# Optimization experiments

Hardware: AMD Instinct MI355X
Metric: run time of the kernel (lower is better)

Reference implementation:

```python
import jax, jax.numpy as jnp
import numpy as np

NEG_INF = -9e15
ALPHA = 0.2  # LeakyReLU slope
ORDER = 2


def gat_layer(x, adj, W, av, concat=True):
    """GraphAttentionLayer forward (eval mode, dropout off).
    x: (b, f, n, t); adj: (b, n, n) int; W: (b, f, c); av: (b, 2c).
    Equivalent to the original repeat_interleave/repeat construction: the
    einsum of 'a' with the (b, 2c, n, m, t) pairwise tensor is linear, so
    e[b,n,m,t] = leakyrelu(a1.Wh[:,n,t] + a2.Wh[:,m,t]).
    """
    Wh = jnp.einsum('bfnt,bfc->bcnt', x, W)            # (b, c, n, t)
    C = Wh.shape[1]
    f1 = jnp.einsum('bcnt,bc->bnt', Wh, av[:, :C])     # source-node term
    f2 = jnp.einsum('bcnt,bc->bnt', Wh, av[:, C:])     # target-node term
    e = jax.nn.leaky_relu(f1[:, :, None, :] + f2[:, None, :, :], ALPHA)  # (b,n,m,t)
    e = jnp.where(adj[:, :, :, None] > 0, e, NEG_INF)
    att = jax.nn.softmax(e, axis=2)                    # softmax over m
    h = jnp.einsum('bnmt,bcmt->bcnt', att, Wh)
    return jax.nn.elu(h) if concat else h


def setup_inputs() -> dict:
    key = jax.random.key(0)
    ks = jax.random.split(key, 8)
    B, F, N, T = 16, 32, 200, 48
    S = 3  # support_len
    c_out = 64
    c_cat = (ORDER * S + 1) * F  # 224
    x = jax.random.normal(ks[0], (B, F, N, T), dtype=jnp.float32)
    support = jax.random.randint(ks[1], (B, S, N, N), 0, 2, dtype=jnp.int32)
    W1 = jax.random.normal(ks[2], (S, B, F, F), dtype=jnp.float32) * (1.414 / np.sqrt(F))
    a1 = jax.random.normal(ks[3], (S, B, 2 * F), dtype=jnp.float32) * 0.1
    WK = jax.random.normal(ks[4], (S * (ORDER - 1), B, F, F), dtype=jnp.float32) * (1.414 / np.sqrt(F))
    aK = jax.random.normal(ks[5], (S * (ORDER - 1), B, 2 * F), dtype=jnp.float32) * 0.1
    mlp_w = jax.random.normal(ks[6], (c_out, c_cat), dtype=jnp.float32) * (1.0 / np.sqrt(c_cat))
    mlp_b = jnp.zeros((c_out,), dtype=jnp.float32)
    return {"x": x, "support": support, "W1": W1, "a1": a1,
            "WK": WK, "aK": aK, "mlp_w": mlp_w, "mlp_b": mlp_b}


def reference(x, support, W1, a1, WK, aK, mlp_w, mlp_b):
    """gcn3 forward (eval mode): multi-hop GAT diffusion + concat + 1x1 conv."""
    S = support.shape[1]
    out = [x]
    count = 0
    for idx in range(S):
        adj = support[:, idx]
        x1 = gat_layer(x, adj, W1[idx], a1[idx])
        out.append(x1)
        for _ in range(2, ORDER + 1):
            x2 = jax.nn.relu(gat_layer(x1, adj, WK[count], aK[count]))
            out.append(x2)
            x1 = x2
            count += 1
    h = jnp.concatenate(out, axis=1)                    # (b, 7*F, n, t)
    h = jnp.einsum('bcnt,oc->bont', h, mlp_w) + mlp_b[None, :, None, None]
    return h
```

## Files before the change

### kernel.cpp

```cpp
#include <hip/hip_runtime.h>
#include <math.h>

#define BB 16
#define FD 32
#define ND 200
#define TD 48
#define SD 3
#define OC 64
#define SLICE 6400
#define TSTRIDE 4915200
#define NEGBIG (-9.0e15f)
#define LOG2E 1.44269504088896340736f

typedef __attribute__((ext_vector_type(8))) short bf16x8;
typedef __attribute__((ext_vector_type(4))) float f32x4;
typedef __attribute__((ext_vector_type(4))) unsigned int u32x4;
typedef __attribute__((ext_vector_type(2))) float f32x2;
typedef __attribute__((ext_vector_type(2))) unsigned int u32x2;

static __device__ __forceinline__ unsigned short f2bf(float f) {
  unsigned u = __builtin_bit_cast(unsigned, f);
  return (unsigned short)((u + 0x8000u) >> 16);
}
static __device__ __forceinline__ unsigned short f2bf_rne(float f) {
  unsigned u = __builtin_bit_cast(unsigned, f);
  return (unsigned short)((u + 0x7FFFu + ((u >> 16) & 1u)) >> 16);
}
static __device__ __forceinline__ float bf2f(unsigned short h) {
  unsigned u = ((unsigned)h) << 16;
  return __builtin_bit_cast(float, u);
}

static __device__ __forceinline__ unsigned int pk_bf16_rhu(float a, float b) {
  unsigned ua = __builtin_bit_cast(unsigned, a) + 0x8000u;
  unsigned ub = __builtin_bit_cast(unsigned, b) + 0x8000u;
#if __has_builtin(__builtin_amdgcn_perm)
  return __builtin_amdgcn_perm(ub, ua, 0x07060302u);
#else
  return (ua >> 16) | (ub & 0xFFFF0000u);
#endif
}

#if __has_builtin(__builtin_amdgcn_exp2f)
static __device__ __forceinline__ float exp2_hw(float x) { return __builtin_amdgcn_exp2f(x); }
#else
static __device__ __forceinline__ float exp2_hw(float x) { return exp2f(x); }
#endif

#if __has_builtin(__builtin_amdgcn_rcpf)
static __device__ __forceinline__ float rcp_hw(float x) { return __builtin_amdgcn_rcpf(x); }
#else
static __device__ __forceinline__ float rcp_hw(float x) { return 1.0f / x; }
#endif

static __device__ __forceinline__ unsigned int sext_bit(unsigned int v, int j) {
#if __has_builtin(__builtin_amdgcn_sbfe)
  return (unsigned int)__builtin_amdgcn_sbfe((int)v, j, 1);
#else
  return 0u - ((v >> j) & 1u);
#endif
}

static __device__ __forceinline__ unsigned int merge_hw(unsigned int lo, unsigned int hi) {
#if __has_builtin(__builtin_amdgcn_perm)
  return __builtin_amdgcn_perm(hi, lo, 0x07060100u);
#else
  return (lo & 0x0000FFFFu) | (hi & 0xFFFF0000u);
#endif
}

__global__ __launch_bounds__(256) void k_prep(
    const float* __restrict__ x, const int* __restrict__ support,
    const float* __restrict__ W1, const float* __restrict__ WK,
    const float* __restrict__ a1, const float* __restrict__ aK,
    const float* __restrict__ mw,
    unsigned short* __restrict__ Xtnc, unsigned short* __restrict__ Xntc,
    unsigned long long* __restrict__ msk,
    unsigned short* __restrict__ Wtb, unsigned short* __restrict__ Wxb,
    unsigned short* __restrict__ mwb) {
  __shared__ float sbuf[3104];
  int bid = blockIdx.x;
  if (bid < 800) {
    int b = bid / 50, n0 = (bid % 50) * 4;
    unsigned short* sf16 = (unsigned short*)sbuf;
    const float4* xv = (const float4*)x;
    for (int i = threadIdx.x; i < 1536; i += 256) {
      int nn = i / 384, rem = i % 384, f = rem / 12, q = rem % 12;
      float4 v = xv[(size_t)((b * 32 + f) * ND + n0 + nn) * 12 + q];
      unsigned short* p = &sf16[f * 194 + nn * 48 + 4 * q];
      p[0] = f2bf(v.x);
      p[1] = f2bf(v.y);
      p[2] = f2bf(v.z);
      p[3] = f2bf(v.w);
    }
    __syncthreads();
    unsigned int* dt = (unsigned int*)Xtnc;
    unsigned int* dn = (unsigned int*)Xntc;
    for (int j = threadIdx.x; j < 3072; j += 256) {
      int t = j >> 6, rem = j & 63, nn = rem >> 4, fq = rem & 15;
      int col = nn * 48 + t;
      unsigned int v = (unsigned int)sf16[(2 * fq) * 194 + col] |
                       ((unsigned int)sf16[(2 * fq + 1) * 194 + col] << 16);
      dt[((size_t)(b * 48 + t) * ND + n0 + nn) * 16 + fq] = v;
    }
    for (int j = threadIdx.x; j < 3072; j += 256) {
      int nn = j / 768, rem = j % 768, t = rem >> 4, fq = rem & 15;
      int col = nn * 48 + t;
      unsigned int v = (unsigned int)sf16[(2 * fq) * 194 + col] |
                       ((unsigned int)sf16[(2 * fq + 1) * 194 + col] << 16);
      dn[((size_t)(b * ND + n0 + nn) * 48 + t) * 16 + fq] = v;
    }
  } else if (bid < 1424) {
    int q = bid - 800;
    int si = q / 13, rg = q % 13;
    const int* adjb = support + (size_t)si * ND * ND;
    int wv = threadIdx.x >> 6, lane = threadIdx.x & 63;
#pragma unroll
    for (int j = 0; j < 4; j++) {
      int r = rg * 16 + wv * 4 + j;
      unsigned long long ws0 = 0, ws1 = 0, ws2 = 0, ws3 = 0;
      if (r < ND) {
        ws0 = __ballot(adjb[r * ND + lane] > 0);
        ws1 = __ballot(adjb[r * ND + 64 + lane] > 0);
        ws2 = __ballot(((128 + lane < ND) ? adjb[r * ND + 128 + lane] : 0) > 0);
        ws3 = __ballot(((192 + lane < ND) ? adjb[r * ND + 192 + lane] : 0) > 0);
      }
      if (lane < 4 && r < 208) {
        unsigned long long o = 0;
#pragma unroll
        for (int k = 0; k < 7; k++) {
          int bidx = k * 4 + lane;
          int sel = bidx >> 3;
          unsigned long long src = (sel == 0) ? ws0 : (sel == 1) ? ws1
                                 : (sel == 2) ? ws2 : ws3;
          unsigned long long byte = (src >> ((bidx & 7) * 8)) & 0xFFull;
          o |= byte << (8 * k);
        }
        msk[((size_t)si * 208 + r) * 4 + lane] = o;
      }
    }
  } else {
    int b2 = bid - 1424;
    if (b2 < 96) {
      int mat = b2 >> 4, b = b2 & 15;
      const float* src = (mat < 3) ? (W1 + (size_t)(mat * 16 + b) * 1024)
                                   : (WK + (size_t)((mat - 3) * 16 + b) * 1024);
      const float* av = (mat < 3) ? (a1 + (size_t)mat * 1024 + b * 64)
                                  : (aK + (size_t)(mat - 3) * 1024 + b * 64);
      unsigned short* dst = Wtb + (size_t)b2 * 1024;
      for (int i = threadIdx.x; i < 1024; i += 256) {
        int c = i >> 5, f = i & 31;
        dst[c * 32 + f] = f2bf_rne(src[f * 32 + c]);
      }
      if (threadIdx.x < 32) {
        int f = threadIdx.x;
        float s1 = 0.f, s2 = 0.f;
        for (int c = 0; c < 32; c++) {
          float wfc = src[f * 32 + c];
          s1 = fmaf(wfc, av[c], s1);
          s2 = fmaf(wfc, av[32 + c], s2);
        }
        sbuf[f] = s1;
        sbuf[32 + f] = s2;
      }
      __syncthreads();
      unsigned short* wx = Wxb + (size_t)b2 * 512;
      for (int i = threadIdx.x; i < 512; i += 256) {
        int col = i >> 5, f = i & 31;
        unsigned short o = 0;
        if (col < 4) {
          float s = sbuf[(col >> 1) * 32 + f];
          unsigned short hi = f2bf_rne(s);
          o = (col & 1) ? f2bf_rne(s - bf2f(hi)) : hi;
        }
        wx[i] = o;
      }
    } else {
      int i = (b2 - 96) * 256 + threadIdx.x;
      if (i < OC * 224) mwb[i] = f2bf_rne(mw[i]);
    }
  }
}

__global__ __launch_bounds__(256) void k_gat2(
    const unsigned short* __restrict__ Xb,
    const unsigned short* __restrict__ Wtb,
    const unsigned short* __restrict__ Wxb,
    const unsigned char* __restrict__ mskb,
    unsigned short* __restrict__ bfp) {
  int bx = blockIdx.x;
  int idx = bx / (BB * TD);
  int bt = bx % (BB * TD);
  int b = bt / TD, t = bt % TD;
  __shared__ __align__(16) unsigned short Vt[32 * 232];
  __shared__ __align__(16) unsigned short Y1s[208 * 32];
  __shared__ __align__(16) unsigned int f2e[224];
  __shared__ __align__(16) float2 f1e[208];
  __shared__ float SVa[64];
  int tid = threadIdx.x, w = tid >> 6, lane = tid & 63;
  int cl = lane & 15, qd = lane >> 4;

  if (tid < 64) SVa[tid] = 0.f;
  for (int i = tid; i < 512; i += 256) {
    int cch = i >> 4, d = i & 15;
    ((unsigned int*)&Vt[cch * 232 + 200])[d] = 0u;
  }
  for (int i = tid; i < 128; i += 256)
    ((unsigned int*)&Y1s[200 * 32])[i] = 0u;
  __syncthreads();

  const unsigned char* mrow = mskb + (size_t)(b * SD + idx) * 208 * 32;
  bf16x8 ones;
#pragma unroll
  for (int j = 0; j < 8; j++) ones[j] = (short)0x3F80;
  size_t xbase = (size_t)bt * SLICE;
  unsigned short* Yb1 = bfp + (size_t)(1 + 2 * idx) * TSTRIDE;
  unsigned short* Yb2 = bfp + (size_t)(2 + 2 * idx) * TSTRIDE;
  const float C1 = LOG2E;
  const float C2 = 0.2f * LOG2E;

#pragma unroll
  for (int hop = 0; hop < 2; hop++) {
    int mat = (hop == 0) ? idx : (3 + idx);
    const unsigned short* wtb = Wtb + (size_t)(mat * 16 + b) * 1024;
    const unsigned short* wxb = Wxb + (size_t)(mat * 16 + b) * 512;
    bf16x8 Bw0 = *(const bf16x8*)(wtb + cl * 32 + qd * 8);
    bf16x8 Bw1 = *(const bf16x8*)(wtb + (cl + 16) * 32 + qd * 8);
    bf16x8 Bwx = *(const bf16x8*)(wxb + cl * 32 + qd * 8);
    float* SV = SVa + hop * 32;

    for (int ti = w; ti < 13; ti += 4) {
      bf16x8 A;
      if (hop == 0)
        A = *(const bf16x8*)(Xb + xbase + (size_t)(ti * 16 + cl) * 32 + qd * 8);
      else
        A = *(const bf16x8*)&Y1s[(ti * 16 + cl) * 32 + qd * 8];
      f32x4 d0 = {0.f, 0.f, 0.f, 0.f}, d1 = d0, d2 = d0;
      d0 = __builtin_amdgcn_mfma_f32_16x16x32_bf16(A, Bw0, d0, 0, 0, 0);
      d1 = __builtin_amdgcn_mfma_f32_16x16x32_bf16(A, Bw1, d1, 0, 0, 0);
      d2 = __builtin_amdgcn_mfma_f32_16x16x32_bf16(A, Bwx, d2, 0, 0, 0);
      int rn0 = ti * 16 + qd * 4;
      float s0 = 0.f, s1 = 0.f;
#pragma unroll
      for (int r = 0; r < 4; r++) {
        float fv = d2[r] + __shfl_xor(d2[r], 1, 64);
        int rn = rn0 + r;
        if (rn < ND) {
          s0 += d0[r];
          s1 += d1[r];
          float E = exp2_hw(fv * C1);
          float Es = exp2_hw(fv * C2);
          if (cl == 0) f1e[rn] = make_float2(E, Es);
          if (cl == 2) f2e[rn] = pk_bf16_rhu(Es, E);
        }
      }
      if (rn0 + 3 < ND) {
        uint2 q0, q1;
        q0.x = pk_bf16_rhu(d0[0], d0[1]);
        q0.y = pk_bf16_rhu(d0[2], d0[3]);
        q1.x = pk_bf16_rhu(d1[0], d1[1]);
        q1.y = pk_bf16_rhu(d1[2], d1[3]);
        *(uint2*)&Vt[cl * 232 + rn0] = q0;
        *(uint2*)&Vt[(cl + 16) * 232 + rn0] = q1;
      }
      atomicAdd(&SV[cl], s0);
      atomicAdd(&SV[cl + 16], s1);
    }
    __syncthreads();

#define ATT_EPI(TI, DEN, AC0, AC1)                                        \
      {                                                                   \
        _Pragma("unroll")                                                 \
        for (int r = 0; r < 4; r++) {                                     \
          int rn = (TI) * 16 + qd * 4 + r;                                \
          if (rn < ND) {                                                  \
            float dn = DEN[r];                                            \
            float v0, v1;                                                 \
            if (dn > 0.f) {                                               \
              float iv = rcp_hw(dn);                                      \
              v0 = AC0[r] * iv;                                           \
              v1 = AC1[r] * iv;                                           \
            } else {                                                      \
              v0 = SV[cl] * (1.0f / ND);                                  \
              v1 = SV[cl + 16] * (1.0f / ND);                             \
            }                                                             \
            if (hop == 0) {                                               \
              v0 = (v0 > 0.f) ? v0 : exp2_hw(v0 * LOG2E) - 1.f;           \
              v1 = (v1 > 0.f) ? v1 : exp2_hw(v1 * LOG2E) - 1.f;           \
            } else {                                                      \
              v0 = fmaxf(v0, 0.f);                                        \
              v1 = fmaxf(v1, 0.f);                                        \
            }                                                             \
            Y1s[rn * 32 + cl] = f2bf(v0);                                 \
            Y1s[rn * 32 + cl + 16] = f2bf(v1);                            \
          }                                                               \
        }                                                                 \
      }

#define ATT_TILE(EE, MB, AW)                                              \
          {                                                               \
            unsigned int mm = merge_hw(sext_bit(MB, 2 * p),               \
                                       sext_bit(MB, 2 * p + 1));          \
            f32x2 pa = EE.x * ehv;                                        \
            f32x2 pb = EE.y * elv;                                        \
            f32x2 pm = __builtin_elementwise_max(pa, pb);                 \
            AW[p] = pk_bf16_rhu(pm.x, pm.y) & mm;                         \
          }

    {
      int r0 = w * 16 + cl, r1 = (w + 4) * 16 + cl, r2 = (w + 8) * 16 + cl;
      float2 e0 = f1e[r0], e1 = f1e[r1], e2 = f1e[r2];
      const unsigned long long mq0 =
          *(const unsigned long long*)(mrow + (size_t)r0 * 32 + qd * 8);
      const unsigned long long mq1 =
          *(const unsigned long long*)(mrow + (size_t)r1 * 32 + qd * 8);
      const unsigned long long mq2 =
          *(const unsigned long long*)(mrow + (size_t)r2 * 32 + qd * 8);
      f32x4 z4 = {0.f, 0.f, 0.f, 0.f};
      f32x4 den0 = z4, den1 = z4, den2 = z4;
      f32x4 a00 = z4, a01 = z4, a02 = z4;
      f32x4 a10 = z4, a11 = z4, a12 = z4;
#pragma unroll
      for (int k = 0; k < 7; k++) {
        int m0 = k * 32 + qd * 8;
        bf16x8 vb0 = *(const bf16x8*)&Vt[cl * 232 + m0];
        bf16x8 vb1 = *(const bf16x8*)&Vt[(cl + 16) * 232 + m0];
        u32x4 ua = *(const u32x4*)&f2e[m0];
        u32x4 ub = *(const u32x4*)&f2e[m0 + 4];
        unsigned int mb0 = (unsigned int)(mq0 >> (8 * k)) & 0xFFu;
        unsigned int mb1 = (unsigned int)(mq1 >> (8 * k)) & 0xFFu;
        unsigned int mb2 = (unsigned int)(mq2 >> (8 * k)) & 0xFFu;
        u32x4 aw0, aw1, aw2;
#pragma unroll
        for (int p = 0; p < 4; p++) {
          unsigned int u0 = (p < 2) ? ((p & 1) ? ua.z : ua.x)
                                    : ((p & 1) ? ub.z : ub.x);
          unsigned int u1 = (p < 2) ? ((p & 1) ? ua.w : ua.y)
                                    : ((p & 1) ? ub.w : ub.y);
          u32x2 uv = {u0, u1};
          f32x2 ehv = __builtin_bit_cast(f32x2, uv & 0xFFFF0000u);
          f32x2 elv = __builtin_bit_cast(f32x2, uv << 16);
          ATT_TILE(e0, mb0, aw0)
          ATT_TILE(e1, mb1, aw1)
          ATT_TILE(e2, mb2, aw2)
        }
        bf16x8 A0 = __builtin_bit_cast(bf16x8, aw0);
        bf16x8 A1 = __builtin_bit_cast(bf16x8, aw1);
        bf16x8 A2 = __builtin_bit_cast(bf16x8, aw2);
        den0 = __builtin_amdgcn_mfma_f32_16x16x32_bf16(A0, ones, den0, 0, 0, 0);
        a00 = __builtin_amdgcn_mfma_f32_16x16x32_bf16(A0, vb0, a00, 0, 0, 0);
        a10 = __builtin_amdgcn_mfma_f32_16x16x32_bf16(A0, vb1, a10, 0, 0, 0);
        den1 = __builtin_amdgcn_mfma_f32_16x16x32_bf16(A1, ones, den1, 0, 0, 0);
        a01 = __builtin_amdgcn_mfma_f32_16x16x32_bf16(A1, vb0, a01, 0, 0, 0);
        a11 = __builtin_amdgcn_mfma_f32_16x16x32_bf16(A1, vb1, a11, 0, 0, 0);
        den2 = __builtin_amdgcn_mfma_f32_16x16x32_bf16(A2, ones, den2, 0, 0, 0);
        a02 = __builtin_amdgcn_mfma_f32_16x16x32_bf16(A2, vb0, a02, 0, 0, 0);
        a12 = __builtin_amdgcn_mfma_f32_16x16x32_bf16(A2, vb1, a12, 0, 0, 0);
      }
      ATT_EPI(w, den0, a00, a10)
      ATT_EPI(w + 4, den1, a01, a11)
      ATT_EPI(w + 8, den2, a02, a12)
    }

    if (w == 0) {
      int r3 = 192 + cl;
      float2 e3 = f1e[r3];
      const unsigned long long mq3 =
          *(const unsigned long long*)(mrow + (size_t)r3 * 32 + qd * 8);
      f32x4 z4 = {0.f, 0.f, 0.f, 0.f};
      f32x4 den3 = z4, a03 = z4, a13 = z4;
#pragma unroll
      for (int k = 0; k < 7; k++) {
        int m0 = k * 32 + qd * 8;
        bf16x8 vb0 = *(const bf16x8*)&Vt[cl * 232 + m0];
        bf16x8 vb1 = *(const bf16x8*)&Vt[(cl + 16) * 232 + m0];
        u32x4 ua = *(const u32x4*)&f2e[m0];
        u32x4 ub = *(const u32x4*)&f2e[m0 + 4];
        unsigned int mb3 = (unsigned int)(mq3 >> (8 * k)) & 0xFFu;
        u32x4 aw3;
#pragma unroll
        for (int p = 0; p < 4; p++) {
          unsigned int u0 = (p < 2) ? ((p & 1) ? ua.z : ua.x)
                                    : ((p & 1) ? ub.z : ub.x);
          unsigned int u1 = (p < 2) ? ((p & 1) ? ua.w : ua.y)
                                    : ((p & 1) ? ub.w : ub.y);
          u32x2 uv = {u0, u1};
          f32x2 ehv = __builtin_bit_cast(f32x2, uv & 0xFFFF0000u);
          f32x2 elv = __builtin_bit_cast(f32x2, uv << 16);
          ATT_TILE(e3, mb3, aw3)
        }
        bf16x8 A3 = __builtin_bit_cast(bf16x8, aw3);
        den3 = __builtin_amdgcn_mfma_f32_16x16x32_bf16(A3, ones, den3, 0, 0, 0);
        a03 = __builtin_amdgcn_mfma_f32_16x16x32_bf16(A3, vb0, a03, 0, 0, 0);
        a13 = __builtin_amdgcn_mfma_f32_16x16x32_bf16(A3, vb1, a13, 0, 0, 0);
      }
      ATT_EPI(12, den3, a03, a13)
    }
#undef ATT_TILE
#undef ATT_EPI
    __syncthreads();
    {
      unsigned short* Yb = (hop == 0) ? Yb1 : Yb2;
      for (int i = tid; i < 800; i += 256) {
        int rn = i >> 2, part = i & 3;
        uint4 vq = *(const uint4*)&Y1s[rn * 32 + part * 8];
        *(uint4*)(Yb + ((size_t)(b * ND + rn) * TD + t) * 32 + part * 8) = vq;
      }
    }
  }
}

__global__ __launch_bounds__(256) void k_conv(
    const unsigned short* __restrict__ hb,
    const unsigned short* __restrict__ mwb,
    const float* __restrict__ mb,
    float* __restrict__ out) {
  int bn = blockIdx.x;
  int b = bn / 100, n0 = (bn % 100) * 2;
  int w = threadIdx.x >> 6, lane = threadIdx.x & 63;
  int cl = lane & 15, qd = lane >> 4;
  bf16x8 bw[7];
#pragma unroll
  for (int k = 0; k < 7; k++)
    bw[k] = *(const bf16x8*)(mwb + (size_t)(w * 16 + cl) * 224 + k * 32 + qd * 8);
  int o = w * 16 + cl;
  float bias = mb[o];
#pragma unroll
  for (int nn = 0; nn < 2; nn++) {
    int n = n0 + nn;
#pragma unroll
    for (int mt = 0; mt < 3; mt++) {
      size_t abase = ((size_t)(b * ND + n) * TD + mt * 16 + cl) * 32 + qd * 8;
      f32x4 acc = {0.f, 0.f, 0.f, 0.f};
#pragma unroll
      for (int k = 0; k < 7; k++) {
        bf16x8 A = *(const bf16x8*)(hb + (size_t)k * TSTRIDE + abase);
        acc = __builtin_amdgcn_mfma_f32_16x16x32_bf16(A, bw[k], acc, 0, 0, 0);
      }
      float4 st;
      st.x = acc[0] + bias;
      st.y = acc[1] + bias;
      st.z = acc[2] + bias;
      st.w = acc[3] + bias;
      *(float4*)(out + ((size_t)(b * OC + o) * ND + n) * TD + mt * 16 + qd * 4) = st;
    }
  }
}

extern "C" void kernel_launch(void* const* d_in, const int* in_sizes, int n_in,
                              void* d_out, int out_size, void* d_ws, size_t ws_size,
                              hipStream_t stream) {
  const float* x = (const float*)d_in[0];
  const int* support = (const int*)d_in[1];
  const float* W1 = (const float*)d_in[2];
  const float* a1 = (const float*)d_in[3];
  const float* WK = (const float*)d_in[4];
  const float* aK = (const float*)d_in[5];
  const float* mw = (const float*)d_in[6];
  const float* mb = (const float*)d_in[7];
  float* out = (float*)d_out;
  char* wsb = (char*)d_ws;
  unsigned short* Xbt = (unsigned short*)wsb;
  unsigned short* bfp = (unsigned short*)(wsb + 9831424);
  unsigned char* msk = (unsigned char*)(wsb + 78644224);
  unsigned short* mwb = (unsigned short*)(wsb + 78963712);
  unsigned short* Wtb = (unsigned short*)(wsb + 78992384);
  unsigned short* Wxb = (unsigned short*)(wsb + 79188992);

  k_prep<<<1576, 256, 0, stream>>>(x, support, W1, WK, a1, aK, mw, Xbt, bfp,
                                   (unsigned long long*)msk, Wtb, Wxb, mwb);
  k_gat2<<<SD * BB * TD, 256, 0, stream>>>(Xbt, Wtb, Wxb, msk, bfp);
  k_conv<<<BB * 100, 256, 0, stream>>>(bfp, mwb, mb, out);
}
```

Before: 222.7 us.

## Precompute expanded 16-bit attention masks and drop the duplicate bf16 x layout

The prep kernel now expands each adjacency bit into a full 16-bit lane mask, stored so the attention kernel can load a u32x4 of ready masks per tile instead of extracting bits with sbfe/perm. It also stops writing the (b,t,n,c) copy of x, and the GAT kernel's first hop reads x from the (b,n,t,c) layout already kept in the concat buffer. This removes one large global write and some per-element ALU work. In exchange the mask buffer grows by about 16x and is read from global memory per tile, and the hop-0 loads become strided across n.

```diff
diff --git a/kernel.cpp b/kernel.cpp
--- a/kernel.cpp
+++ b/kernel.cpp
@@ -53,29 +53,13 @@
 static __device__ __forceinline__ float rcp_hw(float x) { return 1.0f / x; }
 #endif
 
-static __device__ __forceinline__ unsigned int sext_bit(unsigned int v, int j) {
-#if __has_builtin(__builtin_amdgcn_sbfe)
-  return (unsigned int)__builtin_amdgcn_sbfe((int)v, j, 1);
-#else
-  return 0u - ((v >> j) & 1u);
-#endif
-}
-
-static __device__ __forceinline__ unsigned int merge_hw(unsigned int lo, unsigned int hi) {
-#if __has_builtin(__builtin_amdgcn_perm)
-  return __builtin_amdgcn_perm(hi, lo, 0x07060100u);
-#else
-  return (lo & 0x0000FFFFu) | (hi & 0xFFFF0000u);
-#endif
-}
-
 __global__ __launch_bounds__(256) void k_prep(
     const float* __restrict__ x, const int* __restrict__ support,
     const float* __restrict__ W1, const float* __restrict__ WK,
     const float* __restrict__ a1, const float* __restrict__ aK,
     const float* __restrict__ mw,
-    unsigned short* __restrict__ Xtnc, unsigned short* __restrict__ Xntc,
-    unsigned long long* __restrict__ msk,
+    unsigned short* __restrict__ Xntc,
+    unsigned int* __restrict__ emsk,
     unsigned short* __restrict__ Wtb, unsigned short* __restrict__ Wxb,
     unsigned short* __restrict__ mwb) {
   __shared__ float sbuf[3104];
@@ -94,15 +78,7 @@
       p[3] = f2bf(v.w);
     }
     __syncthreads();
-    unsigned int* dt = (unsigned int*)Xtnc;
     unsigned int* dn = (unsigned int*)Xntc;
-    for (int j = threadIdx.x; j < 3072; j += 256) {
-      int t = j >> 6, rem = j & 63, nn = rem >> 4, fq = rem & 15;
-      int col = nn * 48 + t;
-      unsigned int v = (unsigned int)sf16[(2 * fq) * 194 + col] |
-                       ((unsigned int)sf16[(2 * fq + 1) * 194 + col] << 16);
-      dt[((size_t)(b * 48 + t) * ND + n0 + nn) * 16 + fq] = v;
-    }
     for (int j = threadIdx.x; j < 3072; j += 256) {
       int nn = j / 768, rem = j % 768, t = rem >> 4, fq = rem & 15;
       int col = nn * 48 + t;
@@ -114,7 +90,7 @@
     int q = bid - 800;
     int si = q / 13, rg = q % 13;
     const int* adjb = support + (size_t)si * ND * ND;
-    int wv = threadIdx.x >> 6, lane = threadIdx.x & 63;
+    int lane = threadIdx.x & 63, wv = threadIdx.x >> 6;
 #pragma unroll
     for (int j = 0; j < 4; j++) {
       int r = rg * 16 + wv * 4 + j;
@@ -125,18 +101,22 @@
         ws2 = __ballot(((128 + lane < ND) ? adjb[r * ND + 128 + lane] : 0) > 0);
         ws3 = __ballot(((192 + lane < ND) ? adjb[r * ND + 192 + lane] : 0) > 0);
       }
-      if (lane < 4 && r < 208) {
-        unsigned long long o = 0;
-#pragma unroll
-        for (int k = 0; k < 7; k++) {
-          int bidx = k * 4 + lane;
-          int sel = bidx >> 3;
-          unsigned long long src = (sel == 0) ? ws0 : (sel == 1) ? ws1
-                                 : (sel == 2) ? ws2 : ws3;
-          unsigned long long byte = (src >> ((bidx & 7) * 8)) & 0xFFull;
-          o |= byte << (8 * k);
-        }
-        msk[((size_t)si * 208 + r) * 4 + lane] = o;
+      if (r < 208) {
+#pragma unroll
+        for (int half = 0; half < 2; half++) {
+          int w = lane + half * 64;
+          if (w < 112) {
+            int k = w >> 4, rem = w & 15, qdw = rem >> 2, pw = rem & 3;
+            int e0 = k * 32 + qdw * 8 + 2 * pw;
+            int sel = e0 >> 6, sh = e0 & 63;
+            unsigned long long src = (sel == 0) ? ws0 : (sel == 1) ? ws1
+                                   : (sel == 2) ? ws2 : ws3;
+            unsigned b0 = (unsigned)((src >> sh) & 1ull);
+            unsigned b1 = (unsigned)((src >> (sh + 1)) & 1ull);
+            emsk[((size_t)si * 208 + r) * 112 + w] =
+                (b0 * 0xFFFFu) | (b1 * 0xFFFF0000u);
+          }
+        }
       }
     }
   } else {
@@ -183,11 +163,10 @@
 }
 
 __global__ __launch_bounds__(256) void k_gat2(
-    const unsigned short* __restrict__ Xb,
+    unsigned short* __restrict__ bfp,
     const unsigned short* __restrict__ Wtb,
     const unsigned short* __restrict__ Wxb,
-    const unsigned char* __restrict__ mskb,
-    unsigned short* __restrict__ bfp) {
+    const unsigned int* __restrict__ emsk) {
   int bx = blockIdx.x;
   int idx = bx / (BB * TD);
   int bt = bx % (BB * TD);
@@ -209,11 +188,10 @@
     ((unsigned int*)&Y1s[200 * 32])[i] = 0u;
   __syncthreads();
 
-  const unsigned char* mrow = mskb + (size_t)(b * SD + idx) * 208 * 32;
+  const unsigned int* emb = emsk + (size_t)(b * SD + idx) * 208 * 112;
   bf16x8 ones;
 #pragma unroll
   for (int j = 0; j < 8; j++) ones[j] = (short)0x3F80;
-  size_t xbase = (size_t)bt * SLICE;
   unsigned short* Yb1 = bfp + (size_t)(1 + 2 * idx) * TSTRIDE;
   unsigned short* Yb2 = bfp + (size_t)(2 + 2 * idx) * TSTRIDE;
   const float C1 = LOG2E;
@@ -232,7 +210,8 @@
     for (int ti = w; ti < 13; ti += 4) {
       bf16x8 A;
       if (hop == 0)
-        A = *(const bf16x8*)(Xb + xbase + (size_t)(ti * 16 + cl) * 32 + qd * 8);
+        A = *(const bf16x8*)(bfp +
+              ((size_t)(b * ND + ti * 16 + cl) * TD + t) * 32 + qd * 8);
       else
         A = *(const bf16x8*)&Y1s[(ti * 16 + cl) * 32 + qd * 8];
       f32x4 d0 = {0.f, 0.f, 0.f, 0.f}, d1 = d0, d2 = d0;
@@ -297,25 +276,20 @@
         }                                                                 \
       }
 
-#define ATT_TILE(EE, MB, AW)                                              \
+#define ATT_TILE(EE, MMV, AW)                                             \
           {                                                               \
-            unsigned int mm = merge_hw(sext_bit(MB, 2 * p),               \
-                                       sext_bit(MB, 2 * p + 1));          \
             f32x2 pa = EE.x * ehv;                                        \
             f32x2 pb = EE.y * elv;                                        \
             f32x2 pm = __builtin_elementwise_max(pa, pb);                 \
-            AW[p] = pk_bf16_rhu(pm.x, pm.y) & mm;                         \
+            AW[p] = pk_bf16_rhu(pm.x, pm.y) & MMV[p];                     \
           }
 
     {
       int r0 = w * 16 + cl, r1 = (w + 4) * 16 + cl, r2 = (w + 8) * 16 + cl;
       float2 e0 = f1e[r0], e1 = f1e[r1], e2 = f1e[r2];
-      const unsigned long long mq0 =
-          *(const unsigned long long*)(mrow + (size_t)r0 * 32 + qd * 8);
-      const unsigned long long mq1 =
-          *(const unsigned long long*)(mrow + (size_t)r1 * 32 + qd * 8);
-      const unsigned long long mq2 =
-          *(const unsigned long long*)(mrow + (size_t)r2 * 32 + qd * 8);
+      const unsigned int* em0 = emb + (size_t)r0 * 112 + qd * 4;
+      const unsigned int* em1 = emb + (size_t)r1 * 112 + qd * 4;
+      const unsigned int* em2 = emb + (size_t)r2 * 112 + qd * 4;
       f32x4 z4 = {0.f, 0.f, 0.f, 0.f};
       f32x4 den0 = z4, den1 = z4, den2 = z4;
       f32x4 a00 = z4, a01 = z4, a02 = z4;
@@ -327,9 +301,9 @@
         bf16x8 vb1 = *(const bf16x8*)&Vt[(cl + 16) * 232 + m0];
         u32x4 ua = *(const u32x4*)&f2e[m0];
         u32x4 ub = *(const u32x4*)&f2e[m0 + 4];
-        unsigned int mb0 = (unsigned int)(mq0 >> (8 * k)) & 0xFFu;
-        unsigned int mb1 = (unsigned int)(mq1 >> (8 * k)) & 0xFFu;
-        unsigned int mb2 = (unsigned int)(mq2 >> (8 * k)) & 0xFFu;
+        u32x4 mm0 = *(const u32x4*)(em0 + k * 16);
+        u32x4 mm1 = *(const u32x4*)(em1 + k * 16);
+        u32x4 mm2 = *(const u32x4*)(em2 + k * 16);
         u32x4 aw0, aw1, aw2;
 #pragma unroll
         for (int p = 0; p < 4; p++) {
@@ -340,9 +314,9 @@
           u32x2 uv = {u0, u1};
           f32x2 ehv = __builtin_bit_cast(f32x2, uv & 0xFFFF0000u);
           f32x2 elv = __builtin_bit_cast(f32x2, uv << 16);
-          ATT_TILE(e0, mb0, aw0)
-          ATT_TILE(e1, mb1, aw1)
-          ATT_TILE(e2, mb2, aw2)
+          ATT_TILE(e0, mm0, aw0)
+          ATT_TILE(e1, mm1, aw1)
+          ATT_TILE(e2, mm2, aw2)
         }
         bf16x8 A0 = __builtin_bit_cast(bf16x8, aw0);
         bf16x8 A1 = __builtin_bit_cast(bf16x8, aw1);
@@ -365,8 +339,7 @@
     if (w == 0) {
       int r3 = 192 + cl;
       float2 e3 = f1e[r3];
-      const unsigned long long mq3 =
-          *(const unsigned long long*)(mrow + (size_t)r3 * 32 + qd * 8);
+      const unsigned int* em3 = emb + (size_t)r3 * 112 + qd * 4;
       f32x4 z4 = {0.f, 0.f, 0.f, 0.f};
       f32x4 den3 = z4, a03 = z4, a13 = z4;
 #pragma unroll
@@ -376,7 +349,7 @@
         bf16x8 vb1 = *(const bf16x8*)&Vt[(cl + 16) * 232 + m0];
         u32x4 ua = *(const u32x4*)&f2e[m0];
         u32x4 ub = *(const u32x4*)&f2e[m0 + 4];
-        unsigned int mb3 = (unsigned int)(mq3 >> (8 * k)) & 0xFFu;
+        u32x4 mm3 = *(const u32x4*)(em3 + k * 16);
         u32x4 aw3;
 #pragma unroll
         for (int p = 0; p < 4; p++) {
@@ -387,7 +360,7 @@
           u32x2 uv = {u0, u1};
           f32x2 ehv = __builtin_bit_cast(f32x2, uv & 0xFFFF0000u);
           f32x2 elv = __builtin_bit_cast(f32x2, uv << 16);
-          ATT_TILE(e3, mb3, aw3)
+          ATT_TILE(e3, mm3, aw3)
         }
         bf16x8 A3 = __builtin_bit_cast(bf16x8, aw3);
         den3 = __builtin_amdgcn_mfma_f32_16x16x32_bf16(A3, ones, den3, 0, 0, 0);
@@ -460,15 +433,14 @@
   const float* mb = (const float*)d_in[7];
   float* out = (float*)d_out;
   char* wsb = (char*)d_ws;
-  unsigned short* Xbt = (unsigned short*)wsb;
+  unsigned int* emsk = (unsigned int*)wsb;
   unsigned short* bfp = (unsigned short*)(wsb + 9831424);
-  unsigned char* msk = (unsigned char*)(wsb + 78644224);
   unsigned short* mwb = (unsigned short*)(wsb + 78963712);
   unsigned short* Wtb = (unsigned short*)(wsb + 78992384);
   unsigned short* Wxb = (unsigned short*)(wsb + 79188992);
 
-  k_prep<<<1576, 256, 0, stream>>>(x, support, W1, WK, a1, aK, mw, Xbt, bfp,
-                                   (unsigned long long*)msk, Wtb, Wxb, mwb);
-  k_gat2<<<SD * BB * TD, 256, 0, stream>>>(Xbt, Wtb, Wxb, msk, bfp);
+  k_prep<<<1576, 256, 0, stream>>>(x, support, W1, WK, a1, aK, mw, bfp, emsk,
+                                   Wtb, Wxb, mwb);
+  k_gat2<<<SD * BB * TD, 256, 0, stream>>>(bfp, Wtb, Wxb, emsk);
   k_conv<<<BB * 100, 256, 0, stream>>>(bfp, mwb, mb, out);
 }
```

Result: faster. 217.6 us (-2.3%).
